# Performance work log

Hardware: AMD Instinct MI355X
Metric: run time of the kernel (lower is better)

Reference implementation:

```python
import jax, jax.numpy as jnp
import numpy as np

NUM_HEADS = 16


def setup_inputs() -> dict:
    key = jax.random.key(0)
    ks = jax.random.split(key, 4)
    B, S, D = 2, 2048, 1024
    scale = 1.0 / np.sqrt(D)
    x = jax.random.normal(ks[0], (B, S, D), dtype=jnp.float32)
    Wq = jax.random.normal(ks[1], (D, D), dtype=jnp.float32) * scale
    Wk = jax.random.normal(ks[2], (D, D), dtype=jnp.float32) * scale
    Wv = jax.random.normal(ks[3], (D, D), dtype=jnp.float32) * scale
    bq = jnp.zeros((D,), dtype=jnp.float32)
    bk = jnp.zeros((D,), dtype=jnp.float32)
    bv = jnp.zeros((D,), dtype=jnp.float32)
    return {"x": x, "Wq": Wq, "bq": bq, "Wk": Wk, "bk": bk, "Wv": Wv, "bv": bv}


def _split_heads(t, H):
    B, S, D = t.shape
    return t.reshape(B, S, H, D // H).transpose(0, 2, 1, 3)  # (B,H,S,depth)


def reference(x, Wq, bq, Wk, bk, Wv, bv):
    H = NUM_HEADS
    B, S, D = x.shape
    depth = D // H
    q = _split_heads(x @ Wq + bq, H)
    k = _split_heads(x @ Wk + bk, H)
    v = _split_heads(x @ Wv + bv, H)
    # causal mask: strictly-upper-triangular ones, added as finfo.min * mask
    mask = 1.0 - jnp.tril(jnp.ones((S, S), dtype=jnp.float32))
    scores = jnp.einsum("bhqd,bhkd->bhqk", q, k) / jnp.sqrt(jnp.float32(depth))
    scores = scores + jnp.float32(np.finfo(np.float32).min) * mask
    probs = jax.nn.softmax(scores, axis=-1)
    att = jnp.einsum("bhqk,bhkd->bhqd", probs, v)
    return att.transpose(0, 2, 1, 3).reshape(B, S, D)
```

## Files before the change

kernel.cpp:

```cpp
#include <hip/hip_runtime.h>
#include <hip/hip_bf16.h>

#define B_ 2
#define S_ 2048
#define D_ 1024
#define H_ 16
#define DH 64
#define M_ (B_*S_)
#define NT_ (S_/64)

using bf16x8 = __attribute__((ext_vector_type(8))) __bf16;
using f32x4  = __attribute__((ext_vector_type(4))) float;

__device__ __forceinline__ int swz(int row) { return ((row ^ (row >> 3)) & 7) << 3; }

__device__ __forceinline__ void glds16(const __bf16* g, __bf16* l) {
#if __has_builtin(__builtin_amdgcn_global_load_lds)
  __builtin_amdgcn_global_load_lds(
      (const __attribute__((address_space(1))) unsigned int*)g,
      (__attribute__((address_space(3))) unsigned int*)l, 16, 0, 0);
#else
  *(bf16x8*)l = *(const bf16x8*)g;
#endif
}

__global__ __launch_bounds__(256) void conv_x(const float* __restrict__ x,
                                              __bf16* __restrict__ xb) {
  int idx = blockIdx.x * 256 + threadIdx.x;
  int m = idx >> 7, k = (idx & 127) * 8;
  float4 a = *(const float4*)&x[(size_t)m * D_ + k];
  float4 b = *(const float4*)&x[(size_t)m * D_ + k + 4];
  bf16x8 o;
  o[0]=(__bf16)a.x; o[1]=(__bf16)a.y; o[2]=(__bf16)a.z; o[3]=(__bf16)a.w;
  o[4]=(__bf16)b.x; o[5]=(__bf16)b.y; o[6]=(__bf16)b.z; o[7]=(__bf16)b.w;
  *(bf16x8*)&xb[(size_t)m * D_ + (k & ~63) + ((k & 63) ^ swz(m))] = o;
}

__global__ __launch_bounds__(256) void conv_w(const float* __restrict__ Wq,
                                              const float* __restrict__ Wk,
                                              const float* __restrict__ Wv,
                                              __bf16* __restrict__ wt) {
  int z = blockIdx.z;
  const float* __restrict__ W = (z == 0) ? Wq : (z == 1) ? Wk : Wv;
  __bf16* __restrict__ Wt = wt + (size_t)z * D_ * D_;
  __shared__ __bf16 Lt[64 * 66];
  int tid = threadIdx.x;
  int k0 = blockIdx.x * 64, n0 = blockIdx.y * 64;
  #pragma unroll
  for (int i = 0; i < 4; ++i) {
    int f4 = i * 256 + tid;
    int r = f4 >> 4, c4 = (f4 & 15) * 4;
    float4 v = *(const float4*)&W[(size_t)(k0 + r) * D_ + n0 + c4];
    Lt[(c4 + 0) * 66 + r] = (__bf16)v.x;
    Lt[(c4 + 1) * 66 + r] = (__bf16)v.y;
    Lt[(c4 + 2) * 66 + r] = (__bf16)v.z;
    Lt[(c4 + 3) * 66 + r] = (__bf16)v.w;
  }
  __syncthreads();
  #pragma unroll
  for (int i = 0; i < 2; ++i) {
    int idx = i * 256 + tid;
    int n = idx >> 3, kc = (idx & 7) * 8;
    int nf = n0 + n;
    bf16x8 o;
    #pragma unroll
    for (int j = 0; j < 8; ++j) o[j] = Lt[n * 66 + kc + j];
    *(bf16x8*)&Wt[(size_t)nf * D_ + k0 + (kc ^ swz(nf))] = o;
  }
}

#define BM 256
#define BN 256
#define BK 64
#define NKT (D_/BK)

__global__ __launch_bounds__(512) void qkv_gemm(
    const __bf16* __restrict__ xb, const __bf16* __restrict__ wt,
    const float* __restrict__ bq, const float* __restrict__ bk,
    const float* __restrict__ bv, __bf16* __restrict__ qkv) {
  int z = blockIdx.z;
  const __bf16* __restrict__ Wt = wt + (size_t)z * D_ * D_;
  const float* __restrict__ bias = (z == 0) ? bq : (z == 1) ? bk : bv;
  __bf16* __restrict__ out = qkv + (size_t)z * M_ * D_;
  const float scale = (z == 0) ? 0.125f : 1.0f;

  __shared__ __bf16 Al[2][BM * BK];
  __shared__ __bf16 Bl[2][BM * BK];

  int tid = threadIdx.x, lane = tid & 63, w = tid >> 6;
  int m0 = blockIdx.y * BM, n0 = blockIdx.x * BN;
  int wr = (w >> 2) * 128;
  int wc = (w & 3) * 64;

  f32x4 acc[8][4] = {};

#define STAGE(buf, kt)                                                        \
  {                                                                           \
    int k0 = (kt) * BK;                                                       \
    _Pragma("unroll")                                                         \
    for (int r = 0; r < 4; ++r) {                                             \
      int e = (r * 512 + tid) * 8;                                            \
      int row = e >> 6, col = e & 63;                                         \
      glds16(&xb[(size_t)(m0 + row) * D_ + k0 + col], &Al[buf][e]);           \
      glds16(&Wt[(size_t)(n0 + row) * D_ + k0 + col], &Bl[buf][e]);           \
    }                                                                         \
  }

  STAGE(0, 0);
  __syncthreads();

  int cur = 0;
  for (int kt = 0; kt < NKT; ++kt) {
    if (kt + 1 < NKT) STAGE(cur ^ 1, kt + 1);
    #pragma unroll
    for (int kk = 0; kk < 2; ++kk) {
      bf16x8 af[8], bfr[4];
      #pragma unroll
      for (int mi = 0; mi < 8; ++mi) {
        int row = wr + mi * 16 + (lane & 15);
        af[mi] = *(const bf16x8*)&Al[cur][row * 64 +
                 ((kk * 32 + (lane >> 4) * 8) ^ swz(row))];
      }
      #pragma unroll
      for (int ni = 0; ni < 4; ++ni) {
        int col = wc + ni * 16 + (lane & 15);
        bfr[ni] = *(const bf16x8*)&Bl[cur][col * 64 +
                  ((kk * 32 + (lane >> 4) * 8) ^ swz(col))];
      }
      #pragma unroll
      for (int mi = 0; mi < 8; ++mi)
        #pragma unroll
        for (int ni = 0; ni < 4; ++ni)
          acc[mi][ni] = __builtin_amdgcn_mfma_f32_16x16x32_bf16(
              af[mi], bfr[ni], acc[mi][ni], 0, 0, 0);
    }
    __syncthreads();
    cur ^= 1;
  }
#undef STAGE

  #pragma unroll
  for (int mi = 0; mi < 8; ++mi) {
    #pragma unroll
    for (int ni = 0; ni < 4; ++ni) {
      int col = n0 + wc + ni * 16 + (lane & 15);
      int h = col >> 6, dh = col & 63;
      float bv_ = bias[col];
      #pragma unroll
      for (int r = 0; r < 4; ++r) {
        int row = m0 + wr + mi * 16 + (lane >> 4) * 4 + r;
        int b = row >> 11, s = row & 2047;
        out[((size_t)(b * H_ + h) * S_ + s) * DH + dh] =
            (__bf16)((acc[mi][ni][r] + bv_) * scale);
      }
    }
  }
}

__global__ __launch_bounds__(256) void vtrans(const __bf16* __restrict__ v,
                                              __bf16* __restrict__ vt) {
  __shared__ __bf16 Lt[64 * 64];
  int tid = threadIdx.x;
  int s0 = blockIdx.x * 64;
  int h = blockIdx.y, b = blockIdx.z;
  const __bf16* __restrict__ src = v + ((size_t)(b * H_ + h)) * S_ * DH;
  __bf16* __restrict__ dst = vt + ((size_t)(b * H_ + h)) * DH * S_;
  #pragma unroll
  for (int i = 0; i < 2; ++i) {
    int e = (i * 256 + tid) * 8;
    int s = e >> 6, d0 = e & 63;
    bf16x8 r = *(const bf16x8*)&src[(size_t)(s0 + s) * DH + d0];
    #pragma unroll
    for (int j = 0; j < 8; ++j) {
      int d = d0 + j;
      Lt[d * 64 + (s ^ swz(d))] = r[j];
    }
  }
  __syncthreads();
  #pragma unroll
  for (int i = 0; i < 2; ++i) {
    int e = (i * 256 + tid) * 8;
    int d = e >> 6, sc = e & 63;
    bf16x8 o = *(const bf16x8*)&Lt[d * 64 + (sc ^ swz(d))];
    *(bf16x8*)&dst[(size_t)d * S_ + s0 + sc] = o;
  }
}

__device__ __forceinline__ void attn_tile_sw(
    const bf16x8* aq, f32x4* accO, float& m_reg, float& l_reg,
    const __bf16* __restrict__ Kl, const __bf16* __restrict__ Vt,
    __bf16* __restrict__ Plw, int lane, int kv0, int qbase, bool diag) {
  const int g = lane >> 4;
  const int ql = lane & 15;
  f32x4 sfT[4];
  __builtin_amdgcn_s_setprio(1);
  #pragma unroll
  for (int f = 0; f < 4; ++f) {
    f32x4 zz = {};
    int row = f * 16 + ql;
    int sr = swz(row);
    #pragma unroll
    for (int kk = 0; kk < 2; ++kk) {
      bf16x8 ka = *(const bf16x8*)&Kl[row * 64 + ((kk * 32 + g * 8) ^ sr)];
      zz = __builtin_amdgcn_mfma_f32_16x16x32_bf16(ka, aq[kk], zz, 0, 0, 0);
    }
    sfT[f] = zz;
  }
  __builtin_amdgcn_s_setprio(0);

  if (diag) {
    int qg = qbase + ql;
    #pragma unroll
    for (int f = 0; f < 4; ++f)
      #pragma unroll
      for (int r = 0; r < 4; ++r)
        if (kv0 + f * 16 + g * 4 + r > qg) sfT[f][r] = -1e30f;
  }

  float mx = sfT[0][0];
  #pragma unroll
  for (int f = 0; f < 4; ++f)
    #pragma unroll
    for (int r = 0; r < 4; ++r) mx = fmaxf(mx, sfT[f][r]);
  mx = fmaxf(mx, __shfl_xor(mx, 16, 64));
  mx = fmaxf(mx, __shfl_xor(mx, 32, 64));
  float mnew = fmaxf(m_reg, mx);
  float alpha = __expf(m_reg - mnew);
  m_reg = mnew;
  float rs = 0.f;
  #pragma unroll
  for (int f = 0; f < 4; ++f)
    #pragma unroll
    for (int r = 0; r < 4; ++r) {
      float p = __expf(sfT[f][r] - mnew);
      sfT[f][r] = p;
      rs += p;
    }
  rs += __shfl_xor(rs, 16, 64);
  rs += __shfl_xor(rs, 32, 64);
  l_reg = l_reg * alpha + rs;

  const int key = (ql & 7) << 3;
  #pragma unroll
  for (int f = 0; f < 4; ++f)
    #pragma unroll
    for (int r = 0; r < 4; ++r)
      Plw[ql * 64 + ((f * 16 + g * 4 + r) ^ key)] = (__bf16)sfT[f][r];

  float ab[4];
  #pragma unroll
  for (int r = 0; r < 4; ++r) ab[r] = __shfl(alpha, g * 4 + r, 16);
  #pragma unroll
  for (int f = 0; f < 4; ++f)
    #pragma unroll
    for (int r = 0; r < 4; ++r) accO[f][r] *= ab[r];

  __builtin_amdgcn_s_setprio(1);
  #pragma unroll
  for (int kk = 0; kk < 2; ++kk) {
    bf16x8 pa = *(const bf16x8*)&Plw[ql * 64 + ((kk * 32 + g * 8) ^ key)];
    #pragma unroll
    for (int f = 0; f < 4; ++f) {
      int vrow = f * 16 + ql;
      bf16x8 vb = *(const bf16x8*)&Vt[vrow * 64 + ((kk * 32 + g * 8) ^ swz(vrow))];
      accO[f] = __builtin_amdgcn_mfma_f32_16x16x32_bf16(pa, vb, accO[f], 0, 0, 0);
    }
  }
  __builtin_amdgcn_s_setprio(0);
}

__device__ __forceinline__ void attn_out_sw(
    const f32x4* accO, float l_reg, float* __restrict__ out,
    int b, int h, int qbase, int lane) {
  float lr[4];
  #pragma unroll
  for (int r = 0; r < 4; ++r) lr[r] = __shfl(l_reg, (lane >> 4) * 4 + r, 16);
  #pragma unroll
  for (int f = 0; f < 4; ++f) {
    int dh = f * 16 + (lane & 15);
    #pragma unroll
    for (int r = 0; r < 4; ++r) {
      int qg = qbase + (lane >> 4) * 4 + r;
      out[((size_t)(b * S_ + qg)) * D_ + h * DH + dh] = accO[f][r] / lr[r];
    }
  }
}

__global__ __launch_bounds__(256) void attn(
    const __bf16* __restrict__ Q, const __bf16* __restrict__ K,
    const __bf16* __restrict__ VT, float* __restrict__ out) {
  __shared__ __bf16 Kl[64 * 64];
  __shared__ __bf16 Vt[64 * 64];
  __shared__ __bf16 Pl[4][16 * 64];

  int tid = threadIdx.x, lane = tid & 63, w = tid >> 6;
  int bx = blockIdx.x, h = blockIdx.y, b = blockIdx.z;
  int qA0 = bx * 64, qB0 = (NT_ - 1 - bx) * 64;
  size_t base = ((size_t)(b * H_ + h)) * S_ * DH;
  const __bf16* __restrict__ Qg = Q + base;
  const __bf16* __restrict__ Kg = K + base;
  const __bf16* __restrict__ VTg = VT + base;

  bf16x8 aqA[2], aqB[2];
  int qra = qA0 + w * 16 + (lane & 15), qrb = qB0 + w * 16 + (lane & 15);
  #pragma unroll
  for (int kk = 0; kk < 2; ++kk) {
    aqA[kk] = *(const bf16x8*)&Qg[(size_t)qra * DH + kk * 32 + (lane >> 4) * 8];
    aqB[kk] = *(const bf16x8*)&Qg[(size_t)qrb * DH + kk * 32 + (lane >> 4) * 8];
  }

  f32x4 accA[4] = {}, accB[4] = {};
  float mA = -1e30f, lA = 0.f, mB = -1e30f, lB = 0.f;

  const int ktA = bx, ktB = NT_ - 1 - bx;

  bf16x8 kreg[2], vreg[2];
  #pragma unroll
  for (int i = 0; i < 2; ++i) {
    int e = (i * 256 + tid) * 8;
    kreg[i] = *(const bf16x8*)&Kg[(size_t)(e >> 6) * DH + (e & 63)];
    vreg[i] = *(const bf16x8*)&VTg[(size_t)(e >> 6) * S_ + (e & 63)];
  }

  for (int kt = 0; kt <= ktB; ++kt) {
    int kv0 = kt * 64;
    #pragma unroll
    for (int i = 0; i < 2; ++i) {
      int e = (i * 256 + tid) * 8;
      int rrow = e >> 6, cc = e & 63;
      *(bf16x8*)&Kl[rrow * 64 + (cc ^ swz(rrow))] = kreg[i];
      *(bf16x8*)&Vt[rrow * 64 + (cc ^ swz(rrow))] = vreg[i];
    }
    __syncthreads();

    if (kt < ktB) {
      int kvn = kv0 + 64;
      #pragma unroll
      for (int i = 0; i < 2; ++i) {
        int e = (i * 256 + tid) * 8;
        kreg[i] = *(const bf16x8*)&Kg[(size_t)(kvn + (e >> 6)) * DH + (e & 63)];
        vreg[i] = *(const bf16x8*)&VTg[(size_t)(e >> 6) * S_ + kvn + (e & 63)];
      }
    }

    attn_tile_sw(aqB, accB, mB, lB, Kl, Vt, Pl[w], lane, kv0, qB0 + w * 16,
                 kt == ktB);
    if (kt <= ktA)
      attn_tile_sw(aqA, accA, mA, lA, Kl, Vt, Pl[w], lane, kv0, qA0 + w * 16,
                   kt == ktA);
    __syncthreads();
  }

  attn_out_sw(accA, lA, out, b, h, qA0 + w * 16, lane);
  attn_out_sw(accB, lB, out, b, h, qB0 + w * 16, lane);
}

extern "C" void kernel_launch(void* const* d_in, const int* in_sizes, int n_in,
                              void* d_out, int out_size, void* d_ws, size_t ws_size,
                              hipStream_t stream) {
  const float* x  = (const float*)d_in[0];
  const float* Wq = (const float*)d_in[1];
  const float* bq = (const float*)d_in[2];
  const float* Wk = (const float*)d_in[3];
  const float* bk = (const float*)d_in[4];
  const float* Wv = (const float*)d_in[5];
  const float* bv = (const float*)d_in[6];
  float* out = (float*)d_out;

  __bf16* xb  = (__bf16*)d_ws;
  __bf16* wt  = xb + (size_t)M_ * D_;
  __bf16* qkv = wt + (size_t)3 * D_ * D_;
  __bf16* wsq = qkv;
  __bf16* wsk = qkv + (size_t)M_ * D_;
  __bf16* wsv = qkv + (size_t)2 * M_ * D_;
  __bf16* vtg = xb;

  conv_x<<<(M_ * (D_ / 8)) / 256, 256, 0, stream>>>(x, xb);
  conv_w<<<dim3(D_ / 64, D_ / 64, 3), 256, 0, stream>>>(Wq, Wk, Wv, wt);
  qkv_gemm<<<dim3(D_ / BN, M_ / BM, 3), 512, 0, stream>>>(xb, wt, bq, bk, bv, qkv);
  vtrans<<<dim3(S_ / 64, H_, B_), 256, 0, stream>>>(wsv, vtg);
  attn<<<dim3(NT_ / 2, H_, B_), 256, 0, stream>>>(wsq, wsk, vtg, out);
}
```

Before: 189.6 us.

## Fold log2e into Q scale, use exp2, lazy rescale, share K loads across tiles

Q is pre-scaled by log2(e)/8 so softmax can use exp2f directly. The running-max rescale of the accumulator is skipped when no row's max grows by more than a threshold (a lazy-rescale trick). QK^T for both query tiles is computed in one loop that reuses each K fragment read from LDS, and each tile gets its own P buffer. This cuts exp work, rescale multiplies and LDS reads, but the lazy rescale lets exponent values exceed 1 (up to about 2^11.5), which risks bf16 precision loss in P.

```diff
diff --git a/kernel.cpp b/kernel.cpp
--- a/kernel.cpp
+++ b/kernel.cpp
@@ -82,7 +82,7 @@
   const __bf16* __restrict__ Wt = wt + (size_t)z * D_ * D_;
   const float* __restrict__ bias = (z == 0) ? bq : (z == 1) ? bk : bv;
   __bf16* __restrict__ out = qkv + (size_t)z * M_ * D_;
-  const float scale = (z == 0) ? 0.125f : 1.0f;
+  const float scale = (z == 0) ? 0.18033688f : 1.0f;
 
   __shared__ __bf16 Al[2][BM * BK];
   __shared__ __bf16 Bl[2][BM * BK];
@@ -186,27 +186,12 @@
   }
 }
 
-__device__ __forceinline__ void attn_tile_sw(
-    const bf16x8* aq, f32x4* accO, float& m_reg, float& l_reg,
-    const __bf16* __restrict__ Kl, const __bf16* __restrict__ Vt,
-    __bf16* __restrict__ Plw, int lane, int kv0, int qbase, bool diag) {
+__device__ __forceinline__ void smax_pv(
+    f32x4* sfT, f32x4* accO, float& m_reg, float& l_reg,
+    const __bf16* __restrict__ Vt, __bf16* __restrict__ Plw,
+    int lane, int kv0, int qbase, bool diag) {
   const int g = lane >> 4;
   const int ql = lane & 15;
-  f32x4 sfT[4];
-  __builtin_amdgcn_s_setprio(1);
-  #pragma unroll
-  for (int f = 0; f < 4; ++f) {
-    f32x4 zz = {};
-    int row = f * 16 + ql;
-    int sr = swz(row);
-    #pragma unroll
-    for (int kk = 0; kk < 2; ++kk) {
-      bf16x8 ka = *(const bf16x8*)&Kl[row * 64 + ((kk * 32 + g * 8) ^ sr)];
-      zz = __builtin_amdgcn_mfma_f32_16x16x32_bf16(ka, aq[kk], zz, 0, 0, 0);
-    }
-    sfT[f] = zz;
-  }
-  __builtin_amdgcn_s_setprio(0);
 
   if (diag) {
     int qg = qbase + ql;
@@ -217,28 +202,40 @@
         if (kv0 + f * 16 + g * 4 + r > qg) sfT[f][r] = -1e30f;
   }
 
-  float mx = sfT[0][0];
-  #pragma unroll
-  for (int f = 0; f < 4; ++f)
-    #pragma unroll
-    for (int r = 0; r < 4; ++r) mx = fmaxf(mx, sfT[f][r]);
+  float mx = fmaxf(fmaxf(sfT[0][0], sfT[0][1]), fmaxf(sfT[0][2], sfT[0][3]));
+  #pragma unroll
+  for (int f = 1; f < 4; ++f)
+    mx = fmaxf(mx, fmaxf(fmaxf(sfT[f][0], sfT[f][1]),
+                         fmaxf(sfT[f][2], sfT[f][3])));
   mx = fmaxf(mx, __shfl_xor(mx, 16, 64));
   mx = fmaxf(mx, __shfl_xor(mx, 32, 64));
-  float mnew = fmaxf(m_reg, mx);
-  float alpha = __expf(m_reg - mnew);
-  m_reg = mnew;
+
+  if (!__all(mx <= m_reg + 11.54f)) {
+    float mnew = fmaxf(m_reg, mx);
+    float alpha = exp2f(m_reg - mnew);
+    m_reg = mnew;
+    float ab[4];
+    #pragma unroll
+    for (int r = 0; r < 4; ++r) ab[r] = __shfl(alpha, g * 4 + r, 16);
+    #pragma unroll
+    for (int f = 0; f < 4; ++f)
+      #pragma unroll
+      for (int r = 0; r < 4; ++r) accO[f][r] *= ab[r];
+    l_reg *= alpha;
+  }
+
   float rs = 0.f;
   #pragma unroll
   for (int f = 0; f < 4; ++f)
     #pragma unroll
     for (int r = 0; r < 4; ++r) {
-      float p = __expf(sfT[f][r] - mnew);
+      float p = exp2f(sfT[f][r] - m_reg);
       sfT[f][r] = p;
       rs += p;
     }
   rs += __shfl_xor(rs, 16, 64);
   rs += __shfl_xor(rs, 32, 64);
-  l_reg = l_reg * alpha + rs;
+  l_reg += rs;
 
   const int key = (ql & 7) << 3;
   #pragma unroll
@@ -246,14 +243,6 @@
     #pragma unroll
     for (int r = 0; r < 4; ++r)
       Plw[ql * 64 + ((f * 16 + g * 4 + r) ^ key)] = (__bf16)sfT[f][r];
-
-  float ab[4];
-  #pragma unroll
-  for (int r = 0; r < 4; ++r) ab[r] = __shfl(alpha, g * 4 + r, 16);
-  #pragma unroll
-  for (int f = 0; f < 4; ++f)
-    #pragma unroll
-    for (int r = 0; r < 4; ++r) accO[f][r] *= ab[r];
 
   __builtin_amdgcn_s_setprio(1);
   #pragma unroll
@@ -291,7 +280,7 @@
     const __bf16* __restrict__ VT, float* __restrict__ out) {
   __shared__ __bf16 Kl[64 * 64];
   __shared__ __bf16 Vt[64 * 64];
-  __shared__ __bf16 Pl[4][16 * 64];
+  __shared__ __bf16 Pl[4][2][16 * 64];
 
   int tid = threadIdx.x, lane = tid & 63, w = tid >> 6;
   int bx = blockIdx.x, h = blockIdx.y, b = blockIdx.z;
@@ -301,12 +290,14 @@
   const __bf16* __restrict__ Kg = K + base;
   const __bf16* __restrict__ VTg = VT + base;
 
+  const int g = lane >> 4, ql = lane & 15;
+
   bf16x8 aqA[2], aqB[2];
-  int qra = qA0 + w * 16 + (lane & 15), qrb = qB0 + w * 16 + (lane & 15);
+  int qra = qA0 + w * 16 + ql, qrb = qB0 + w * 16 + ql;
   #pragma unroll
   for (int kk = 0; kk < 2; ++kk) {
-    aqA[kk] = *(const bf16x8*)&Qg[(size_t)qra * DH + kk * 32 + (lane >> 4) * 8];
-    aqB[kk] = *(const bf16x8*)&Qg[(size_t)qrb * DH + kk * 32 + (lane >> 4) * 8];
+    aqA[kk] = *(const bf16x8*)&Qg[(size_t)qra * DH + kk * 32 + g * 8];
+    aqB[kk] = *(const bf16x8*)&Qg[(size_t)qrb * DH + kk * 32 + g * 8];
   }
 
   f32x4 accA[4] = {}, accB[4] = {};
@@ -343,11 +334,28 @@
       }
     }
 
-    attn_tile_sw(aqB, accB, mB, lB, Kl, Vt, Pl[w], lane, kv0, qB0 + w * 16,
-                 kt == ktB);
-    if (kt <= ktA)
-      attn_tile_sw(aqA, accA, mA, lA, Kl, Vt, Pl[w], lane, kv0, qA0 + w * 16,
-                   kt == ktA);
+    const bool doA = (kt <= ktA);
+    f32x4 sB[4], sA[4];
+    __builtin_amdgcn_s_setprio(1);
+    #pragma unroll
+    for (int f = 0; f < 4; ++f) {
+      f32x4 zb = {}, za = {};
+      int row = f * 16 + ql;
+      int sr = swz(row);
+      #pragma unroll
+      for (int kk = 0; kk < 2; ++kk) {
+        bf16x8 ka = *(const bf16x8*)&Kl[row * 64 + ((kk * 32 + g * 8) ^ sr)];
+        zb = __builtin_amdgcn_mfma_f32_16x16x32_bf16(ka, aqB[kk], zb, 0, 0, 0);
+        if (doA)
+          za = __builtin_amdgcn_mfma_f32_16x16x32_bf16(ka, aqA[kk], za, 0, 0, 0);
+      }
+      sB[f] = zb; sA[f] = za;
+    }
+    __builtin_amdgcn_s_setprio(0);
+
+    smax_pv(sB, accB, mB, lB, Vt, Pl[w][0], lane, kv0, qB0 + w * 16, kt == ktB);
+    if (doA)
+      smax_pv(sA, accA, mA, lA, Vt, Pl[w][1], lane, kv0, qA0 + w * 16, kt == ktA);
     __syncthreads();
   }
 
```

Result: slower. 193.6 us (+2.1%).

## Fuse V transpose into GEMM epilogue, merge conversion kernels, remap GEMM grid

Applied to the files above, without the earlier changes.

Merges the x and weight bf16 conversion kernels into one launch. It writes V directly in transposed layout from the QKV GEMM epilogue, eliminating the separate vtrans kernel and its extra memory pass. It also flattens the GEMM grid with an interleaved block-to-tile mapping for locality. The transposed V stores are strided and uncoalesced, which may cost epilogue bandwidth.

```diff
diff --git a/kernel.cpp b/kernel.cpp
--- a/kernel.cpp
+++ b/kernel.cpp
@@ -24,28 +24,30 @@
 #endif
 }
 
-__global__ __launch_bounds__(256) void conv_x(const float* __restrict__ x,
-                                              __bf16* __restrict__ xb) {
-  int idx = blockIdx.x * 256 + threadIdx.x;
-  int m = idx >> 7, k = (idx & 127) * 8;
-  float4 a = *(const float4*)&x[(size_t)m * D_ + k];
-  float4 b = *(const float4*)&x[(size_t)m * D_ + k + 4];
-  bf16x8 o;
-  o[0]=(__bf16)a.x; o[1]=(__bf16)a.y; o[2]=(__bf16)a.z; o[3]=(__bf16)a.w;
-  o[4]=(__bf16)b.x; o[5]=(__bf16)b.y; o[6]=(__bf16)b.z; o[7]=(__bf16)b.w;
-  *(bf16x8*)&xb[(size_t)m * D_ + (k & ~63) + ((k & 63) ^ swz(m))] = o;
-}
-
-__global__ __launch_bounds__(256) void conv_w(const float* __restrict__ Wq,
-                                              const float* __restrict__ Wk,
-                                              const float* __restrict__ Wv,
-                                              __bf16* __restrict__ wt) {
-  int z = blockIdx.z;
+#define NBX 2048
+__global__ __launch_bounds__(256) void prep(
+    const float* __restrict__ x, const float* __restrict__ Wq,
+    const float* __restrict__ Wk, const float* __restrict__ Wv,
+    __bf16* __restrict__ xb, __bf16* __restrict__ wt) {
+  int bid = blockIdx.x, tid = threadIdx.x;
+  if (bid < NBX) {
+    int idx = bid * 256 + tid;
+    int m = idx >> 7, k = (idx & 127) * 8;
+    float4 a = *(const float4*)&x[(size_t)m * D_ + k];
+    float4 b = *(const float4*)&x[(size_t)m * D_ + k + 4];
+    bf16x8 o;
+    o[0]=(__bf16)a.x; o[1]=(__bf16)a.y; o[2]=(__bf16)a.z; o[3]=(__bf16)a.w;
+    o[4]=(__bf16)b.x; o[5]=(__bf16)b.y; o[6]=(__bf16)b.z; o[7]=(__bf16)b.w;
+    *(bf16x8*)&xb[(size_t)m * D_ + (k & ~63) + ((k & 63) ^ swz(m))] = o;
+    return;
+  }
+  int wb = bid - NBX;
+  int z = wb >> 8;
+  int kt = (wb & 255) >> 4, nt = wb & 15;
   const float* __restrict__ W = (z == 0) ? Wq : (z == 1) ? Wk : Wv;
   __bf16* __restrict__ Wt = wt + (size_t)z * D_ * D_;
   __shared__ __bf16 Lt[64 * 66];
-  int tid = threadIdx.x;
-  int k0 = blockIdx.x * 64, n0 = blockIdx.y * 64;
+  int k0 = kt * 64, n0 = nt * 64;
   #pragma unroll
   for (int i = 0; i < 4; ++i) {
     int f4 = i * 256 + tid;
@@ -73,22 +75,28 @@
 #define BN 256
 #define BK 64
 #define NKT (D_/BK)
+#define NWG 192
 
 __global__ __launch_bounds__(512) void qkv_gemm(
     const __bf16* __restrict__ xb, const __bf16* __restrict__ wt,
     const float* __restrict__ bq, const float* __restrict__ bk,
-    const float* __restrict__ bv, __bf16* __restrict__ qkv) {
-  int z = blockIdx.z;
+    const float* __restrict__ bv, __bf16* __restrict__ qk,
+    __bf16* __restrict__ vt) {
+  int flat = blockIdx.x;
+  int sid = (flat & 7) * (NWG / 8) + (flat >> 3);
+  int z = sid >> 6;
+  int rem = sid & 63;
+  int my = rem >> 2, nx = rem & 3;
+
   const __bf16* __restrict__ Wt = wt + (size_t)z * D_ * D_;
   const float* __restrict__ bias = (z == 0) ? bq : (z == 1) ? bk : bv;
-  __bf16* __restrict__ out = qkv + (size_t)z * M_ * D_;
   const float scale = (z == 0) ? 0.125f : 1.0f;
 
   __shared__ __bf16 Al[2][BM * BK];
   __shared__ __bf16 Bl[2][BM * BK];
 
   int tid = threadIdx.x, lane = tid & 63, w = tid >> 6;
-  int m0 = blockIdx.y * BM, n0 = blockIdx.x * BN;
+  int m0 = my * BM, n0 = nx * BN;
   int wr = (w >> 2) * 128;
   int wc = (w & 3) * 64;
 
@@ -139,50 +147,41 @@
   }
 #undef STAGE
 
-  #pragma unroll
-  for (int mi = 0; mi < 8; ++mi) {
-    #pragma unroll
-    for (int ni = 0; ni < 4; ++ni) {
-      int col = n0 + wc + ni * 16 + (lane & 15);
-      int h = col >> 6, dh = col & 63;
-      float bv_ = bias[col];
-      #pragma unroll
-      for (int r = 0; r < 4; ++r) {
-        int row = m0 + wr + mi * 16 + (lane >> 4) * 4 + r;
-        int b = row >> 11, s = row & 2047;
-        out[((size_t)(b * H_ + h) * S_ + s) * DH + dh] =
-            (__bf16)((acc[mi][ni][r] + bv_) * scale);
-      }
-    }
-  }
-}
-
-__global__ __launch_bounds__(256) void vtrans(const __bf16* __restrict__ v,
-                                              __bf16* __restrict__ vt) {
-  __shared__ __bf16 Lt[64 * 64];
-  int tid = threadIdx.x;
-  int s0 = blockIdx.x * 64;
-  int h = blockIdx.y, b = blockIdx.z;
-  const __bf16* __restrict__ src = v + ((size_t)(b * H_ + h)) * S_ * DH;
-  __bf16* __restrict__ dst = vt + ((size_t)(b * H_ + h)) * DH * S_;
-  #pragma unroll
-  for (int i = 0; i < 2; ++i) {
-    int e = (i * 256 + tid) * 8;
-    int s = e >> 6, d0 = e & 63;
-    bf16x8 r = *(const bf16x8*)&src[(size_t)(s0 + s) * DH + d0];
-    #pragma unroll
-    for (int j = 0; j < 8; ++j) {
-      int d = d0 + j;
-      Lt[d * 64 + (s ^ swz(d))] = r[j];
-    }
-  }
-  __syncthreads();
-  #pragma unroll
-  for (int i = 0; i < 2; ++i) {
-    int e = (i * 256 + tid) * 8;
-    int d = e >> 6, sc = e & 63;
-    bf16x8 o = *(const bf16x8*)&Lt[d * 64 + (sc ^ swz(d))];
-    *(bf16x8*)&dst[(size_t)d * S_ + s0 + sc] = o;
+  if (z < 2) {
+    __bf16* __restrict__ out = qk + (size_t)z * M_ * D_;
+    #pragma unroll
+    for (int mi = 0; mi < 8; ++mi) {
+      #pragma unroll
+      for (int ni = 0; ni < 4; ++ni) {
+        int col = n0 + wc + ni * 16 + (lane & 15);
+        int h = col >> 6, dh = col & 63;
+        float bv_ = bias[col];
+        #pragma unroll
+        for (int r = 0; r < 4; ++r) {
+          int row = m0 + wr + mi * 16 + (lane >> 4) * 4 + r;
+          int b = row >> 11, s = row & 2047;
+          out[((size_t)(b * H_ + h) * S_ + s) * DH + dh] =
+              (__bf16)((acc[mi][ni][r] + bv_) * scale);
+        }
+      }
+    }
+  } else {
+    #pragma unroll
+    for (int mi = 0; mi < 8; ++mi) {
+      #pragma unroll
+      for (int ni = 0; ni < 4; ++ni) {
+        int col = n0 + wc + ni * 16 + (lane & 15);
+        int h = col >> 6, dh = col & 63;
+        float bv_ = bias[col];
+        #pragma unroll
+        for (int r = 0; r < 4; ++r) {
+          int row = m0 + wr + mi * 16 + (lane >> 4) * 4 + r;
+          int b = row >> 11, s = row & 2047;
+          vt[((size_t)(b * H_ + h) * DH + dh) * S_ + s] =
+              (__bf16)(acc[mi][ni][r] + bv_);
+        }
+      }
+    }
   }
 }
 
@@ -301,12 +300,14 @@
   const __bf16* __restrict__ Kg = K + base;
   const __bf16* __restrict__ VTg = VT + base;
 
+  const int g = lane >> 4, ql = lane & 15;
+
   bf16x8 aqA[2], aqB[2];
-  int qra = qA0 + w * 16 + (lane & 15), qrb = qB0 + w * 16 + (lane & 15);
+  int qra = qA0 + w * 16 + ql, qrb = qB0 + w * 16 + ql;
   #pragma unroll
   for (int kk = 0; kk < 2; ++kk) {
-    aqA[kk] = *(const bf16x8*)&Qg[(size_t)qra * DH + kk * 32 + (lane >> 4) * 8];
-    aqB[kk] = *(const bf16x8*)&Qg[(size_t)qrb * DH + kk * 32 + (lane >> 4) * 8];
+    aqA[kk] = *(const bf16x8*)&Qg[(size_t)qra * DH + kk * 32 + g * 8];
+    aqB[kk] = *(const bf16x8*)&Qg[(size_t)qrb * DH + kk * 32 + g * 8];
   }
 
   f32x4 accA[4] = {}, accB[4] = {};
@@ -372,12 +373,9 @@
   __bf16* qkv = wt + (size_t)3 * D_ * D_;
   __bf16* wsq = qkv;
   __bf16* wsk = qkv + (size_t)M_ * D_;
-  __bf16* wsv = qkv + (size_t)2 * M_ * D_;
-  __bf16* vtg = xb;
-
-  conv_x<<<(M_ * (D_ / 8)) / 256, 256, 0, stream>>>(x, xb);
-  conv_w<<<dim3(D_ / 64, D_ / 64, 3), 256, 0, stream>>>(Wq, Wk, Wv, wt);
-  qkv_gemm<<<dim3(D_ / BN, M_ / BM, 3), 512, 0, stream>>>(xb, wt, bq, bk, bv, qkv);
-  vtrans<<<dim3(S_ / 64, H_, B_), 256, 0, stream>>>(wsv, vtg);
+  __bf16* vtg = qkv + (size_t)2 * M_ * D_;
+
+  prep<<<NBX + 768, 256, 0, stream>>>(x, Wq, Wk, Wv, xb, wt);
+  qkv_gemm<<<NWG, 512, 0, stream>>>(xb, wt, bq, bk, bv, qkv, vtg);
   attn<<<dim3(NT_ / 2, H_, B_), 256, 0, stream>>>(wsq, wsk, vtg, out);
 }
```

Measured after the change: 183.6 us. 3.2% less time.
